# Kernel tuning notes

Hardware: AMD Instinct MI355X
Metric: run time of the kernel (lower is better)

## Reference

```python
import jax, jax.numpy as jnp
import numpy as np

EPS_TINY = np.float32(np.finfo(np.float32).tiny)  # torch clamp min in continuous_topk


def layernorm(x, gamma, beta, eps=1e-6):
    mu = jnp.mean(x, axis=-1, keepdims=True)
    var = jnp.mean((x - mu) ** 2, axis=-1, keepdims=True)
    return (x - mu) * jax.lax.rsqrt(var + eps) * gamma + beta


def continuous_topk(w, k, t=0.1):
    """Iterative differentiable top-k with hard straight-through, as in the torch code.
    w: (B, N) logits. Returns khot: (B, k, N)."""
    n = w.shape[-1]

    def step(carry, _):
        logits, onehot = carry
        # khot_mask = clamp(1 - onehot, min=EPS); logits accumulate log-mask in place
        logits = logits + jnp.log(jnp.maximum(1.0 - onehot, EPS_TINY))
        soft = jax.nn.softmax(logits / t, axis=-1)
        hard = jax.nn.one_hot(jnp.argmax(soft, axis=-1), n, dtype=soft.dtype)
        st = hard - jax.lax.stop_gradient(soft) + soft  # straight-through
        return (logits, st), st

    (_, _), khot = jax.lax.scan(step, (w, jnp.zeros_like(w)), None, length=k)
    return jnp.transpose(khot, (1, 0, 2))  # (k,B,N) -> (B,k,N)


def setup_inputs():
    key = jax.random.key(0)
    ks = jax.random.split(key, 8)
    B, N, C, COUT = 8, 2048, 256, 256
    s = 0.02
    return {
        "xyzs": jax.random.normal(ks[0], (B, N, 3), jnp.float32),
        "features": jax.random.normal(ks[1], (B, C, N), jnp.float32),
        "ln_gamma": jnp.ones((C,), jnp.float32),
        "ln_beta": jnp.zeros((C,), jnp.float32),
        "Wu1": jax.random.normal(ks[2], (C, C), jnp.float32) * s,
        "bu1": jnp.zeros((C,), jnp.float32),
        "Wu2": jax.random.normal(ks[3], (C, COUT), jnp.float32) * s,
        "bu2": jnp.zeros((COUT,), jnp.float32),
        "Wd1": jax.random.normal(ks[4], (C, C), jnp.float32) * s,
        "bd1": jnp.zeros((C,), jnp.float32),
        "Wd2": jax.random.normal(ks[5], (C, 1), jnp.float32) * s,
        "bd2": jnp.zeros((1,), jnp.float32),
        "out_num_points": 1024,
    }


def reference(xyzs, features, ln_gamma, ln_beta, Wu1, bu1, Wu2, bu2, Wd1, bd1, Wd2, bd2, out_num_points):
    # eval mode: dropout inactive, gumbel_keys skipped (self.training False)
    f = jnp.transpose(features, (0, 2, 1))           # (B, N, C)
    f = layernorm(f, ln_gamma, ln_beta)
    new_f = jnp.maximum(f @ Wu1 + bu1, 0.0) @ Wu2 + bu2   # (B, N, COUT)
    w = (jnp.maximum(f @ Wd1 + bd1, 0.0) @ Wd2 + bd2)[:, :, 0]  # (B, N)
    khot = continuous_topk(w, out_num_points, t=0.1)  # (B, K, N)
    xyzs_out = khot @ xyzs                            # (B, K, 3)
    feats = jnp.einsum('bkn,bnc->bkc', khot, new_f)   # (B, K, COUT)
    indices = jnp.argmax(khot, axis=2)                # (B, K)
    return xyzs_out, jnp.transpose(feats, (0, 2, 1)), indices
```

## Files before the change

### kernel.cpp

```cpp
#include <hip/hip_runtime.h>

#define B_DIM 8
#define N_DIM 2048
#define C_DIM 256
#define K_SEL 1024

typedef __attribute__((ext_vector_type(8))) short short8;
typedef __attribute__((ext_vector_type(4))) float f32x4;

__device__ __forceinline__ unsigned int bf16rne(float x) {
  unsigned int u = __float_as_uint(x);
  return (u + 0x7fffu + ((u >> 16) & 1u)) >> 16;
}

__global__ void __launch_bounds__(256) ln_wgemm(
    const float* __restrict__ feat, const float* __restrict__ gamma,
    const float* __restrict__ beta, float* __restrict__ fbuf,
    const float* __restrict__ Wd1, const float* __restrict__ bd1,
    const float* __restrict__ Wd2, const float* __restrict__ bd2,
    float* __restrict__ wkey) {
  __shared__ __align__(16) float tile[256 * 32];
  __shared__ __align__(16) char smem2[2304 + 16640];
  __shared__ float murs[64];
  __shared__ float gb[512];
  float (*As)[36] = (float (*)[36])smem2;
  float (*Bs)[260] = (float (*)[260])(smem2 + 2304);
  float* H = tile;

  const int t = threadIdx.x;
  const int m0 = blockIdx.x << 5;
  const int b = m0 >> 11, n0 = m0 & 2047;

  gb[t] = gamma[t];
  gb[256 + t] = beta[t];

  const int cg = t >> 3, nl4 = (t & 7) << 2;
  for (int pass = 0; pass < 8; ++pass) {
    const int c = (pass << 5) + cg;
    const float4 v = *(const float4*)(feat + (((long)((b << 8) + c)) << 11) + n0 + nl4);
    const int sw = c & 31;
    float* row = tile + (c << 5);
    row[(nl4 + 0) ^ sw] = v.x; row[(nl4 + 1) ^ sw] = v.y;
    row[(nl4 + 2) ^ sw] = v.z; row[(nl4 + 3) ^ sw] = v.w;
  }
  __syncthreads();

  if (t < 32) {
    float acc = tile[t];
    for (int c = 1; c < 256; ++c) acc = __fadd_rn(acc, tile[(c << 5) + (t ^ (c & 31))]);
    const float mu = __fdiv_rn(acc, 256.0f);

    float pw[2];
#pragma unroll
    for (int blk = 0; blk < 2; ++blk) {
      const int c0 = blk << 7;
      float r8[8];
#pragma unroll
      for (int j = 0; j < 8; ++j) {
        float d = __fsub_rn(tile[((c0 + j) << 5) + (t ^ ((c0 + j) & 31))], mu);
        r8[j] = __fmul_rn(d, d);
      }
      for (int i = 8; i < 128; i += 8) {
#pragma unroll
        for (int j = 0; j < 8; ++j) {
          const int c = c0 + i + j;
          float d = __fsub_rn(tile[(c << 5) + (t ^ (c & 31))], mu);
          r8[j] = __fadd_rn(r8[j], __fmul_rn(d, d));
        }
      }
      pw[blk] = __fadd_rn(__fadd_rn(__fadd_rn(r8[0], r8[1]), __fadd_rn(r8[2], r8[3])),
                          __fadd_rn(__fadd_rn(r8[4], r8[5]), __fadd_rn(r8[6], r8[7])));
    }
    const float var = __fdiv_rn(__fadd_rn(pw[0], pw[1]), 256.0f);
    const float rs = __fdiv_rn(1.0f, __fsqrt_rn(__fadd_rn(var, 1e-6f)));
    murs[t] = mu;
    murs[32 + t] = rs;
  }
  __syncthreads();

  {
    const int c = t;
    const float gac = gb[c], bec = gb[256 + c];
    const float* trow = tile + (c << 5);
    const int sw = c & 31;
    for (int r = 0; r < 32; ++r) {
      const float x = trow[r ^ sw];
      const float o = __fadd_rn(
          __fmul_rn(__fmul_rn(__fsub_rn(x, murs[r]), murs[32 + r]), gac), bec);
      fbuf[(((long)(m0 + r)) << 8) + c] = o;
    }
  }

  const int rowT = t >> 6, colT = t & 63;
  const int ar = t & 31, kg4 = (t >> 5) << 2;
  const int bk = t >> 4, bc = (t & 15) << 4;
  const float mu_a = murs[ar], rs_a = murs[32 + ar];
  float acc[8][4] = {};

  for (int k0 = 0; k0 < 256; k0 += 16) {
    if (t < 128) {
#pragma unroll
      for (int q = 0; q < 4; ++q) {
        const int c = k0 + kg4 + q;
        const float x = tile[(c << 5) + (ar ^ (c & 31))];
        As[kg4 + q][ar] = __fadd_rn(
            __fmul_rn(__fmul_rn(__fsub_rn(x, mu_a), rs_a), gb[c]), gb[256 + c]);
      }
    }
    {
      const float* brow = Wd1 + (((k0 + bk) << 8) + bc);
      *(float4*)&Bs[bk][bc]      = *(const float4*)brow;
      *(float4*)&Bs[bk][bc + 4]  = *(const float4*)(brow + 4);
      *(float4*)&Bs[bk][bc + 8]  = *(const float4*)(brow + 8);
      *(float4*)&Bs[bk][bc + 12] = *(const float4*)(brow + 12);
    }
    __syncthreads();
#pragma unroll
    for (int kk = 0; kk < 16; ++kk) {
      const float4 a0 = *(const float4*)&As[kk][rowT << 3];
      const float4 a1 = *(const float4*)&As[kk][(rowT << 3) + 4];
      const float4 bq = *(const float4*)&Bs[kk][colT << 2];
      const float aa[8] = {a0.x, a0.y, a0.z, a0.w, a1.x, a1.y, a1.z, a1.w};
      const float bbv[4] = {bq.x, bq.y, bq.z, bq.w};
#pragma unroll
      for (int i = 0; i < 8; ++i)
#pragma unroll
        for (int j = 0; j < 4; ++j)
          acc[i][j] = __fmaf_rn(aa[i], bbv[j], acc[i][j]);
    }
    __syncthreads();
  }

  const float4 bd = *(const float4*)(bd1 + (colT << 2));
  const float ba[4] = {bd.x, bd.y, bd.z, bd.w};
#pragma unroll
  for (int i = 0; i < 8; ++i) {
    const int m = (rowT << 3) + i;
#pragma unroll
    for (int j = 0; j < 4; ++j) {
      const int c = (colT << 2) + j;
      H[(c << 5) + (m ^ ((c >> 2) & 31))] = fmaxf(__fadd_rn(acc[i][j], ba[j]), 0.0f);
    }
  }
  __syncthreads();

  if (t < 32) {
    float wa = 0.0f;
    for (int c = 0; c < 256; ++c)
      wa = __fmaf_rn(H[(c << 5) + (t ^ ((c >> 2) & 31))], Wd2[c], wa);
    const float w = __fadd_rn(wa, bd2[0]);
    wkey[m0 + t] = __fdiv_rn(w, 0.1f);
  }
}

__global__ void __launch_bounds__(1024) topk_kernel(
    const float* __restrict__ wv, const float* __restrict__ xyzs,
    int* __restrict__ idx_out, float* __restrict__ out_xyz,
    float* __restrict__ out_idx) {
  __shared__ unsigned long long vals[2048];
  const int b = blockIdx.x, t = threadIdx.x;
#pragma unroll
  for (int h = 0; h < 2; ++h) {
    const int i = (h << 10) + t;
    const unsigned int u = __float_as_uint(wv[(b << 11) + i]);
    const unsigned int up = ((int)u < 0) ? ~u : (u | 0x80000000u);
    vals[i] = (((unsigned long long)(~up)) << 32) | (unsigned int)i;
  }
  __syncthreads();
  for (int k = 2; k <= 2048; k <<= 1) {
    for (int j = k >> 1; j > 0; j >>= 1) {
      for (int half = 0; half < 2; ++half) {
        const int i = (half << 10) | t;
        const int ixj = i ^ j;
        if (ixj > i) {
          const unsigned long long vi = vals[i], vj = vals[ixj];
          const bool up = ((i & k) == 0);
          if ((vi > vj) == up) { vals[i] = vj; vals[ixj] = vi; }
        }
      }
      __syncthreads();
    }
  }
  const int sel = (int)(vals[t] & 0xffffffffu);
  idx_out[(b << 10) + t] = sel;
  out_idx[(b << 10) + t] = (float)sel;
  const long o = ((long)((b << 10) + t)) * 3;
  const long s3 = ((long)((b << 11) + sel)) * 3;
  out_xyz[o] = xyzs[s3]; out_xyz[o + 1] = xyzs[s3 + 1]; out_xyz[o + 2] = xyzs[s3 + 2];
}

__global__ __launch_bounds__(256) void prep_w2(const float* __restrict__ W1,
    const float* __restrict__ W2, unsigned short* __restrict__ P1,
    unsigned short* __restrict__ P2) {
  const int g = blockIdx.x;
  const float* W = (g < 8) ? W1 : W2;
  unsigned short* P = (g < 8) ? P1 : P2;
  const int kc = g & 7, n = threadIdx.x;
  unsigned int packed[16];
#pragma unroll
  for (int i = 0; i < 16; ++i) {
    const float a = W[(((kc << 5) + 2 * i) << 8) + n];
    const float bq = W[(((kc << 5) + 2 * i + 1) << 8) + n];
    packed[i] = bf16rne(a) | (bf16rne(bq) << 16);
  }
  uint4* dst = (uint4*)(P + (((kc << 8) + n) << 5));
#pragma unroll
  for (int q = 0; q < 4; ++q)
    dst[q] = make_uint4(packed[4 * q], packed[4 * q + 1], packed[4 * q + 2], packed[4 * q + 3]);
}

#define APITCH 264
#define BPITCH 40
__global__ void __launch_bounds__(256) up_mfma(
    const float* __restrict__ fbuf, const int* __restrict__ idxm,
    const unsigned short* __restrict__ Wu1P, const float* __restrict__ bu1,
    const unsigned short* __restrict__ Wu2P, const float* __restrict__ bu2,
    float* __restrict__ out_feat) {
  __shared__ __align__(16) char smem[32 * APITCH * 2 + 256 * BPITCH * 2 + 64 * 34 * 4 + 2048];
  unsigned short* As = (unsigned short*)smem;
  unsigned short* Bs = (unsigned short*)(smem + 32 * APITCH * 2);
  float* T = (float*)(smem + 32 * APITCH * 2 + 256 * BPITCH * 2);
  float* bias1 = (float*)(smem + 32 * APITCH * 2 + 256 * BPITCH * 2 + 64 * 34 * 4);
  float* bias2 = bias1 + 256;

  const int t = threadIdx.x;
  const int m0 = blockIdx.x << 5;
  const int quad = (t >> 4) & 3, ln = t & 15, w = t >> 6;
  const int rb = w >> 1, ch = w & 1;

  bias1[t] = bu1[t];
  bias2[t] = bu2[t];

  {
    const int r = t & 31, cseg = t >> 5;
    const int m = m0 + r;
    const long srow = (long)(((m >> 10) << 11) + idxm[m]) << 8;
    const float* src = fbuf + srow + (cseg << 5);
    unsigned short* dst = As + r * APITCH + (cseg << 5);
#pragma unroll
    for (int u = 0; u < 8; ++u) {
      const float4 v = *(const float4*)(src + (u << 2));
      const unsigned int lo = bf16rne(v.x) | (bf16rne(v.y) << 16);
      const unsigned int hi = bf16rne(v.z) | (bf16rne(v.w) << 16);
      *(uint2*)(dst + (u << 2)) = make_uint2(lo, hi);
    }
  }

  f32x4 acc[8];
#pragma unroll
  for (int i = 0; i < 8; ++i) acc[i] = (f32x4){0.f, 0.f, 0.f, 0.f};

  for (int kc = 0; kc < 8; ++kc) {
    __syncthreads();
    const uint4* sb = (const uint4*)(Wu1P + (((kc << 8) + t) << 5));
    uint4* db = (uint4*)(Bs + t * BPITCH);
    db[0] = sb[0]; db[1] = sb[1]; db[2] = sb[2]; db[3] = sb[3];
    __syncthreads();
    const short8 a = *(const short8*)(As + ((rb << 4) + ln) * APITCH + (kc << 5) + (quad << 3));
#pragma unroll
    for (int nt = 0; nt < 8; ++nt) {
      const int ntg = (ch << 3) + nt;
      const short8 b = *(const short8*)(Bs + ((ntg << 4) + ln) * BPITCH + (quad << 3));
      acc[nt] = __builtin_amdgcn_mfma_f32_16x16x32_bf16(a, b, acc[nt], 0, 0, 0);
    }
  }

  __syncthreads();
  unsigned short* Hs = As;
#pragma unroll
  for (int nt = 0; nt < 8; ++nt) {
    const int c = ((ch << 3) + nt << 4) + ln;
    const float bb = bias1[c];
#pragma unroll
    for (int rr = 0; rr < 4; ++rr) {
      const float h = fmaxf(acc[nt][rr] + bb, 0.0f);
      Hs[((rb << 4) + (quad << 2) + rr) * APITCH + c] = (unsigned short)bf16rne(h);
    }
  }
#pragma unroll
  for (int i = 0; i < 8; ++i) acc[i] = (f32x4){0.f, 0.f, 0.f, 0.f};

  for (int kc = 0; kc < 8; ++kc) {
    __syncthreads();
    const uint4* sb = (const uint4*)(Wu2P + (((kc << 8) + t) << 5));
    uint4* db = (uint4*)(Bs + t * BPITCH);
    db[0] = sb[0]; db[1] = sb[1]; db[2] = sb[2]; db[3] = sb[3];
    __syncthreads();
    const short8 a = *(const short8*)(Hs + ((rb << 4) + ln) * APITCH + (kc << 5) + (quad << 3));
#pragma unroll
    for (int nt = 0; nt < 8; ++nt) {
      const int ntg = (ch << 3) + nt;
      const short8 b = *(const short8*)(Bs + ((ntg << 4) + ln) * BPITCH + (quad << 3));
      acc[nt] = __builtin_amdgcn_mfma_f32_16x16x32_bf16(a, b, acc[nt], 0, 0, 0);
    }
  }

  const int bb = m0 >> 10, kbase = m0 & 1023;
  for (int ci = 0; ci < 4; ++ci) {
    __syncthreads();
    if ((ci >> 1) == ch) {
#pragma unroll
      for (int q = 0; q < 4; ++q) {
        const int nt = ((ci & 1) << 2) + q;
        const int cloc = (q << 4) + ln;
        const float b2 = bias2[(ci << 6) + cloc];
        const int row = (rb << 4) + (quad << 2);
#pragma unroll
        for (int rr = 0; rr < 4; ++rr)
          T[cloc * 34 + row + rr] = acc[nt][rr] + b2;
      }
    }
    __syncthreads();
#pragma unroll
    for (int p = 0; p < 8; ++p) {
      const int cl = (p << 3) + (t >> 5);
      const int m = t & 31;
      out_feat[((long)((bb << 8) + (ci << 6) + cl) << 10) + kbase + m] = T[cl * 34 + m];
    }
  }
}

extern "C" void kernel_launch(void* const* d_in, const int* in_sizes, int n_in,
                              void* d_out, int out_size, void* d_ws, size_t ws_size,
                              hipStream_t stream) {
  const float* xyzs     = (const float*)d_in[0];
  const float* features = (const float*)d_in[1];
  const float* ln_gamma = (const float*)d_in[2];
  const float* ln_beta  = (const float*)d_in[3];
  const float* Wu1      = (const float*)d_in[4];
  const float* bu1      = (const float*)d_in[5];
  const float* Wu2      = (const float*)d_in[6];
  const float* bu2      = (const float*)d_in[7];
  const float* Wd1      = (const float*)d_in[8];
  const float* bd1      = (const float*)d_in[9];
  const float* Wd2      = (const float*)d_in[10];
  const float* bd2      = (const float*)d_in[11];

  char* ws = (char*)d_ws;
  float* fbuf = (float*)ws;
  unsigned short* Wu1P = (unsigned short*)(ws + 33554432);
  unsigned short* Wu2P = (unsigned short*)(ws + 33685504);
  float* wv   = (float*)(ws + 50331648);
  int*   idx  = (int*)(ws + 50397184);

  float* out_xyz  = (float*)d_out;
  float* out_feat = out_xyz + 24576;
  float* out_idx  = out_feat + 2097152;

  prep_w2<<<16, 256, 0, stream>>>(Wu1, Wu2, Wu1P, Wu2P);
  ln_wgemm<<<512, 256, 0, stream>>>(features, ln_gamma, ln_beta, fbuf,
                                    Wd1, bd1, Wd2, bd2, wv);
  topk_kernel<<<8, 1024, 0, stream>>>(wv, xyzs, idx, out_xyz, out_idx);
  up_mfma<<<256, 256, 0, stream>>>(fbuf, idx, Wu1P, bu1, Wu2P, bu2, out_feat);
}
```

Before: 179.6 us.

## Register-resident bitonic sort with wave shuffles; fold weight prep into LN kernel

The top-k bitonic sort now holds two elements per thread in registers. Partners within a 64-lane wave are exchanged with shuffles, and shared memory plus barriers are used only for strides of 128 or more. This removes most of the per-step __syncthreads and LDS round trips. Separately, the bf16 weight-packing kernel is merged into ln_wgemm as 16 extra blocks, which removes one kernel launch. The sort logic is reworked, so correctness depends on the pairing and direction math matching the original network.

```diff
diff --git a/kernel.cpp b/kernel.cpp
--- a/kernel.cpp
+++ b/kernel.cpp
@@ -18,7 +18,9 @@
     const float* __restrict__ beta, float* __restrict__ fbuf,
     const float* __restrict__ Wd1, const float* __restrict__ bd1,
     const float* __restrict__ Wd2, const float* __restrict__ bd2,
-    float* __restrict__ wkey) {
+    float* __restrict__ wkey,
+    const float* __restrict__ Wu1, const float* __restrict__ Wu2,
+    unsigned short* __restrict__ Wu1P, unsigned short* __restrict__ Wu2P) {
   __shared__ __align__(16) float tile[256 * 32];
   __shared__ __align__(16) char smem2[2304 + 16640];
   __shared__ float murs[64];
@@ -28,6 +30,26 @@
   float* H = tile;
 
   const int t = threadIdx.x;
+
+  if (blockIdx.x >= 512) {
+    const int g = blockIdx.x - 512;
+    const float* W = (g < 8) ? Wu1 : Wu2;
+    unsigned short* P = (g < 8) ? Wu1P : Wu2P;
+    const int kc = g & 7, n = t;
+    unsigned int packed[16];
+#pragma unroll
+    for (int i = 0; i < 16; ++i) {
+      const float a = W[(((kc << 5) + 2 * i) << 8) + n];
+      const float bq = W[(((kc << 5) + 2 * i + 1) << 8) + n];
+      packed[i] = bf16rne(a) | (bf16rne(bq) << 16);
+    }
+    uint4* dst = (uint4*)(P + (((kc << 8) + n) << 5));
+#pragma unroll
+    for (int q = 0; q < 4; ++q)
+      dst[q] = make_uint4(packed[4 * q], packed[4 * q + 1], packed[4 * q + 2], packed[4 * q + 3]);
+    return;
+  }
+
   const int m0 = blockIdx.x << 5;
   const int b = m0 >> 11, n0 = m0 & 2047;
 
@@ -159,54 +181,59 @@
     float* __restrict__ out_idx) {
   __shared__ unsigned long long vals[2048];
   const int b = blockIdx.x, t = threadIdx.x;
-#pragma unroll
-  for (int h = 0; h < 2; ++h) {
-    const int i = (h << 10) + t;
-    const unsigned int u = __float_as_uint(wv[(b << 11) + i]);
-    const unsigned int up = ((int)u < 0) ? ~u : (u | 0x80000000u);
-    vals[i] = (((unsigned long long)(~up)) << 32) | (unsigned int)i;
-  }
-  __syncthreads();
+
+  unsigned long long a0, a1;
+  {
+    const float2 w2 = *(const float2*)(wv + (b << 11) + (t << 1));
+    const unsigned int u0 = __float_as_uint(w2.x);
+    const unsigned int p0 = ((int)u0 < 0) ? ~u0 : (u0 | 0x80000000u);
+    a0 = (((unsigned long long)(~p0)) << 32) | (unsigned int)(2 * t);
+    const unsigned int u1 = __float_as_uint(w2.y);
+    const unsigned int p1 = ((int)u1 < 0) ? ~u1 : (u1 | 0x80000000u);
+    a1 = (((unsigned long long)(~p1)) << 32) | (unsigned int)(2 * t + 1);
+  }
+
   for (int k = 2; k <= 2048; k <<= 1) {
-    for (int j = k >> 1; j > 0; j >>= 1) {
-      for (int half = 0; half < 2; ++half) {
-        const int i = (half << 10) | t;
-        const int ixj = i ^ j;
-        if (ixj > i) {
-          const unsigned long long vi = vals[i], vj = vals[ixj];
-          const bool up = ((i & k) == 0);
-          if ((vi > vj) == up) { vals[i] = vj; vals[ixj] = vi; }
-        }
-      }
-      __syncthreads();
-    }
-  }
-  const int sel = (int)(vals[t] & 0xffffffffu);
-  idx_out[(b << 10) + t] = sel;
-  out_idx[(b << 10) + t] = (float)sel;
-  const long o = ((long)((b << 10) + t)) * 3;
-  const long s3 = ((long)((b << 11) + sel)) * 3;
-  out_xyz[o] = xyzs[s3]; out_xyz[o + 1] = xyzs[s3 + 1]; out_xyz[o + 2] = xyzs[s3 + 2];
-}
-
-__global__ __launch_bounds__(256) void prep_w2(const float* __restrict__ W1,
-    const float* __restrict__ W2, unsigned short* __restrict__ P1,
-    unsigned short* __restrict__ P2) {
-  const int g = blockIdx.x;
-  const float* W = (g < 8) ? W1 : W2;
-  unsigned short* P = (g < 8) ? P1 : P2;
-  const int kc = g & 7, n = threadIdx.x;
-  unsigned int packed[16];
-#pragma unroll
-  for (int i = 0; i < 16; ++i) {
-    const float a = W[(((kc << 5) + 2 * i) << 8) + n];
-    const float bq = W[(((kc << 5) + 2 * i + 1) << 8) + n];
-    packed[i] = bf16rne(a) | (bf16rne(bq) << 16);
-  }
-  uint4* dst = (uint4*)(P + (((kc << 8) + n) << 5));
-#pragma unroll
-  for (int q = 0; q < 4; ++q)
-    dst[q] = make_uint4(packed[4 * q], packed[4 * q + 1], packed[4 * q + 2], packed[4 * q + 3]);
+    for (int j = k >> 1; j >= 2; j >>= 1) {
+      const int x = j >> 1;
+      const bool up = (((t << 1) & k) == 0);
+      unsigned long long p0, p1;
+      if (j >= 128) {
+        vals[2 * t] = a0; vals[2 * t + 1] = a1;
+        __syncthreads();
+        p0 = vals[(2 * t) ^ j];
+        p1 = vals[(2 * t + 1) ^ j];
+        __syncthreads();
+      } else {
+        p0 = __shfl_xor(a0, x, 64);
+        p1 = __shfl_xor(a1, x, 64);
+      }
+      const bool lower = ((t & x) == 0);
+      const bool take_min = (lower == up);
+      a0 = take_min ? (a0 < p0 ? a0 : p0) : (a0 > p0 ? a0 : p0);
+      a1 = take_min ? (a1 < p1 ? a1 : p1) : (a1 > p1 ? a1 : p1);
+    }
+    {
+      const bool up1 = (((t << 1) & k) == 0);
+      if ((a0 > a1) == up1) { const unsigned long long tmp = a0; a0 = a1; a1 = tmp; }
+    }
+  }
+
+  if (t < 512) {
+    const int r0 = 2 * t, r1 = 2 * t + 1;
+    const int s0 = (int)(a0 & 0xffffffffu);
+    const int s1 = (int)(a1 & 0xffffffffu);
+    idx_out[(b << 10) + r0] = s0;
+    idx_out[(b << 10) + r1] = s1;
+    out_idx[(b << 10) + r0] = (float)s0;
+    out_idx[(b << 10) + r1] = (float)s1;
+    const long o0 = ((long)((b << 10) + r0)) * 3;
+    const long q0 = ((long)((b << 11) + s0)) * 3;
+    out_xyz[o0] = xyzs[q0]; out_xyz[o0 + 1] = xyzs[q0 + 1]; out_xyz[o0 + 2] = xyzs[q0 + 2];
+    const long o1 = ((long)((b << 10) + r1)) * 3;
+    const long q1 = ((long)((b << 11) + s1)) * 3;
+    out_xyz[o1] = xyzs[q1]; out_xyz[o1 + 1] = xyzs[q1 + 1]; out_xyz[o1 + 2] = xyzs[q1 + 2];
+  }
 }
 
 #define APITCH 264
@@ -347,9 +374,9 @@
   float* out_feat = out_xyz + 24576;
   float* out_idx  = out_feat + 2097152;
 
-  prep_w2<<<16, 256, 0, stream>>>(Wu1, Wu2, Wu1P, Wu2P);
-  ln_wgemm<<<512, 256, 0, stream>>>(features, ln_gamma, ln_beta, fbuf,
-                                    Wd1, bd1, Wd2, bd2, wv);
+  ln_wgemm<<<528, 256, 0, stream>>>(features, ln_gamma, ln_beta, fbuf,
+                                    Wd1, bd1, Wd2, bd2, wv,
+                                    Wu1, Wu2, Wu1P, Wu2P);
   topk_kernel<<<8, 1024, 0, stream>>>(wv, xyzs, idx, out_xyz, out_idx);
   up_mfma<<<256, 256, 0, stream>>>(fbuf, idx, Wu1P, bu1, Wu2P, bu2, out_feat);
 }
```

Measured after the change: 169.7 us (median of 2 runs). 5.5% less time.
